# Kernel optimization log

Hardware: AMD Instinct MI355X
Metric: run time of the kernel (lower is better)

Reference implementation:

```python
import jax, jax.numpy as jnp
import numpy as np

B, N, D = 64, 4096, 256      # batch, num_inputs, in_features
S, K, H = 11, 128, 256       # num_slots, slot_size, mlp_hidden_size
ITERS = 3
EPS = 1e-6
LN_EPS = 1e-5


def layer_norm(x, w, b):
    m = jnp.mean(x, axis=-1, keepdims=True)
    v = jnp.mean(jnp.square(x - m), axis=-1, keepdims=True)
    return (x - m) * jax.lax.rsqrt(v + LN_EPS) * w + b


def setup_inputs() -> dict:
    key = jax.random.key(0)
    ks = jax.random.split(key, 24)
    rn = lambda i, shape, sc=1.0: jax.random.normal(ks[i], shape, jnp.float32) * sc
    p = 0.05  # param init scale
    return {
        "inputs": rn(0, (B, N, D)),
        "slots_init": rn(1, (B, S, K)),
        "slots_mu": rn(2, (1, 1, K), p),
        "slots_log_sigma": rn(3, (1, 1, K), p),
        "ln_in_w": 1.0 + rn(4, (D,), p), "ln_in_b": rn(5, (D,), p),
        "ln_slot_w": 1.0 + rn(6, (K,), p), "ln_slot_b": rn(7, (K,), p),
        "ln_mlp_w": 1.0 + rn(8, (K,), p), "ln_mlp_b": rn(9, (K,), p),
        "Wq": rn(10, (K, K), p),
        "Wk": rn(11, (K, D), p),
        "Wv": rn(12, (K, D), p),
        "w_ih": rn(13, (3 * K, K), p), "w_hh": rn(14, (3 * K, K), p),
        "b_ih": rn(15, (3 * K,), p), "b_hh": rn(16, (3 * K,), p),
        "mlp_w1": rn(17, (H, K), p), "mlp_b1": rn(18, (H,), p),
        "mlp_w2": rn(19, (K, H), p), "mlp_b2": rn(20, (K,), p),
    }


def reference(inputs, slots_init, slots_mu, slots_log_sigma,
              ln_in_w, ln_in_b, ln_slot_w, ln_slot_b, ln_mlp_w, ln_mlp_b,
              Wq, Wk, Wv, w_ih, w_hh, b_ih, b_hh,
              mlp_w1, mlp_b1, mlp_w2, mlp_b2):
    x = layer_norm(inputs, ln_in_w, ln_in_b)            # [B,N,D]
    k = jnp.einsum('bnd,kd->bnk', x, Wk)                # [B,N,K]
    v = jnp.einsum('bnd,kd->bnk', x, Wv)                # [B,N,K]
    slots = slots_mu + jnp.exp(slots_log_sigma) * slots_init  # [B,S,K]
    scale = K ** -0.5
    for _ in range(ITERS):
        slots_prev = slots
        sn = layer_norm(slots, ln_slot_w, ln_slot_b)
        q = jnp.einsum('bsk,jk->bsj', sn, Wq)           # [B,S,K]
        logits = scale * jnp.einsum('bnk,bsk->bns', k, q)  # [B,N,S]
        attn = jax.nn.softmax(logits, axis=-1) + EPS    # softmax over slots
        attn = attn / jnp.sum(attn, axis=1, keepdims=True)  # renorm over inputs
        updates = jnp.einsum('bns,bnk->bsk', attn, v)   # [B,S,K]
        # GRUCell: input=updates, hidden=slots_prev
        gi = jnp.einsum('bsk,jk->bsj', updates, w_ih) + b_ih     # [B,S,3K]
        gh = jnp.einsum('bsk,jk->bsj', slots_prev, w_hh) + b_hh  # [B,S,3K]
        i_r, i_z, i_n = jnp.split(gi, 3, axis=-1)
        h_r, h_z, h_n = jnp.split(gh, 3, axis=-1)
        r = jax.nn.sigmoid(i_r + h_r)
        z = jax.nn.sigmoid(i_z + h_z)
        n = jnp.tanh(i_n + r * h_n)
        slots = (1.0 - z) * n + z * slots_prev
        m = layer_norm(slots, ln_mlp_w, ln_mlp_b)
        hid = jax.nn.relu(jnp.einsum('bsk,hk->bsh', m, mlp_w1) + mlp_b1)
        slots = slots + jnp.einsum('bsh,kh->bsk', hid, mlp_w2) + mlp_b2
    return slots
```

## Files before the change

kernel.cpp:

```cpp
#include <hip/hip_runtime.h>
#include <hip/hip_bf16.h>
#include <cstdint>
#include <cstddef>

#define B_ 64
#define N_ 4096
#define D_ 256
#define S_ 11
#define K_ 128
#define H_ 256
#define ITERS_ 3
#define EPS_ 1e-6f
#define LN_EPS_ 1e-5f
#define SCALE_ 0.08838834764831845f
#define NCH_ 16

typedef __bf16 bf16x8 __attribute__((ext_vector_type(8)));
typedef float  f32x4  __attribute__((ext_vector_type(4)));

__device__ __forceinline__ unsigned short f2bu(float f) {
  __bf16 h = (__bf16)f;
  return __builtin_bit_cast(unsigned short, h);
}
__device__ __forceinline__ unsigned int pk2(float a, float b) {
  return (unsigned int)f2bu(a) | ((unsigned int)f2bu(b) << 16);
}

__global__ __launch_bounds__(256) void kprep(const float* __restrict__ Wk,
                                             const float* __restrict__ Wv,
                                             const float* __restrict__ lnw,
                                             const float* __restrict__ lnb,
                                             unsigned short* __restrict__ W2pk,
                                             float* __restrict__ c1c2,
                                             const float* __restrict__ si,
                                             const float* __restrict__ mu,
                                             const float* __restrict__ ls,
                                             float* __restrict__ slots,
                                             const float* __restrict__ w_ih,
                                             const float* __restrict__ w_hh,
                                             float* __restrict__ wTih,
                                             float* __restrict__ wThh,
                                             const float* __restrict__ w1,
                                             float* __restrict__ w1T,
                                             const float* __restrict__ w2,
                                             float* __restrict__ w2T,
                                             const float* __restrict__ Wq,
                                             float* __restrict__ WqT) {
  int bid = blockIdx.x, t = threadIdx.x;
  if (bid < 32) {
    int f = bid * 256 + t;
    int ln_ = f & 63, jj = (f >> 6) & 3, kk2 = (f >> 8) & 1, kt = (f >> 9) & 3, ww = f >> 11;
    int row = ww * 64 + jj * 16 + (ln_ & 15);
    int col = kt * 64 + kk2 * 32 + (ln_ >> 4) * 8;
    const float* src = (row < 128) ? (Wk + row * 256 + col) : (Wv + (row - 128) * 256 + col);
    float4 a = *(const float4*)src;
    float4 b = *(const float4*)(src + 4);
    float4 l0 = *(const float4*)(lnw + col);
    float4 l1 = *(const float4*)(lnw + col + 4);
    a.x *= l0.x; a.y *= l0.y; a.z *= l0.z; a.w *= l0.w;
    b.x *= l1.x; b.y *= l1.y; b.z *= l1.z; b.w *= l1.w;
    uint4 u;
    u.x = pk2(a.x, a.y); u.y = pk2(a.z, a.w); u.z = pk2(b.x, b.y); u.w = pk2(b.z, b.w);
    *(uint4*)(W2pk + (size_t)f * 8) = u;
  } else if (bid < 384) {
    int i = (bid - 32) * 256 + t;
    int k = i & 127;
    slots[i] = mu[k] + __expf(ls[k]) * si[i];
  } else if (bid < 576) {
    int i = (bid - 384) * 256 + t;
    int r = i >> 7, c = i & 127;
    wTih[c * 384 + r] = w_ih[i];
  } else if (bid < 768) {
    int i = (bid - 576) * 256 + t;
    int r = i >> 7, c = i & 127;
    wThh[c * 384 + r] = w_hh[i];
  } else if (bid < 896) {
    int i = (bid - 768) * 256 + t;
    int r = i >> 7, c = i & 127;
    w1T[c * 256 + r] = w1[i];
  } else if (bid < 1024) {
    int i = (bid - 896) * 256 + t;
    int r = i >> 8, c = i & 255;
    w2T[c * 128 + r] = w2[i];
  } else if (bid < 1088) {
    int i = (bid - 1024) * 256 + t;
    int r = i >> 7, c = i & 127;
    WqT[c * 128 + r] = Wq[i];
  } else {
    int j = t;
    const float* wrow = (j < 128) ? (Wk + j * 256) : (Wv + (j - 128) * 256);
    float c1 = 0.f, c2 = 0.f;
    for (int d = 0; d < 256; d++) {
      float wv = wrow[d];
      c1 += lnb[d] * wv;
      c2 += lnw[d] * wv;
    }
    c1c2[2 * j] = c1;
    c1c2[2 * j + 1] = c2;
  }
}

__global__ __launch_bounds__(256) void k12_lngemm(const float* __restrict__ x,
                                                  const float* __restrict__ c1c2,
                                                  const unsigned short* __restrict__ W2pk,
                                                  unsigned short* __restrict__ k_frag,
                                                  unsigned short* __restrict__ v_frag) {
  __shared__ char smem[32768];
  __shared__ float2 mu_a[64];
  __shared__ float2 ccs[256];
  const int t = threadIdx.x;
  const int lane = t & 63, w = t >> 6;
  const long rowg0 = (long)blockIdx.x * 64;

  ccs[t] = ((const float2*)c1c2)[t];

  bf16x8 bA[4], bB[4];
  auto loadB = [&](int kt, int kk, bf16x8* dst) {
#pragma unroll
    for (int jl = 0; jl < 4; jl++)
      dst[jl] = *(const bf16x8*)(W2pk +
          (size_t)((w << 11) | (kt << 9) | (kk << 8) | (jl << 6) | lane) * 8);
  };
  loadB(0, 0, bA);

  {
    const float* xb = x + (rowg0 + w * 16) * 256 + lane * 4;
#pragma unroll
    for (int rr = 0; rr < 16; rr++) {
      float4 xv = *(const float4*)(xb + rr * 256);
      int r = w * 16 + rr;
      uint2 pk;
      pk.x = pk2(xv.x, xv.y);
      pk.y = pk2(xv.z, xv.w);
      *(uint2*)(smem + r * 512 + (((lane >> 1) ^ (r & 7)) << 4) + ((lane & 1) << 3)) = pk;
    }
  }
  __syncthreads();

  {
    const int sr = t >> 2, squad = t & 3;
    float s = 0.f, ss = 0.f;
#pragma unroll
    for (int c8 = 0; c8 < 8; c8++) {
      bf16x8 v = *(const bf16x8*)(smem + sr * 512 + ((((squad * 8 + c8) ^ (sr & 7))) << 4));
#pragma unroll
      for (int e = 0; e < 8; e++) {
        float f = (float)v[e];
        s += f; ss += f * f;
      }
    }
    s += __shfl_xor(s, 1);  s += __shfl_xor(s, 2);
    ss += __shfl_xor(ss, 1); ss += __shfl_xor(ss, 2);
    if (squad == 0) {
      float m = s * (1.f / 256.f);
      float var = ss * (1.f / 256.f) - m * m;
      float2 ma; ma.x = m; ma.y = rsqrtf(var + LN_EPS_);
      mu_a[sr] = ma;
    }
  }

  f32x4 acc[4][4] = {};
#pragma unroll
  for (int sstep = 0; sstep < 8; sstep++) {
    const int kt = sstep >> 1, kk = sstep & 1;
    const bf16x8* cur = (sstep & 1) ? bB : bA;
    bf16x8* nxt = (sstep & 1) ? bA : bB;
    if (sstep < 7) loadB((sstep + 1) >> 1, (sstep + 1) & 1, nxt);
    bf16x8 xf[4];
#pragma unroll
    for (int i = 0; i < 4; i++) {
      int row = i * 16 + (lane & 15);
      int slot = (kt * 8 + kk * 4 + (lane >> 4)) ^ (lane & 7);
      xf[i] = *(const bf16x8*)(smem + row * 512 + (slot << 4));
    }
    if (w < 2) {
#pragma unroll
      for (int i = 0; i < 4; i++)
#pragma unroll
        for (int jl = 0; jl < 4; jl++)
          acc[i][jl] = __builtin_amdgcn_mfma_f32_16x16x32_bf16(cur[jl], xf[i], acc[i][jl], 0, 0, 0);
    } else {
#pragma unroll
      for (int i = 0; i < 4; i++)
#pragma unroll
        for (int jl = 0; jl < 4; jl++)
          acc[i][jl] = __builtin_amdgcn_mfma_f32_16x16x32_bf16(xf[i], cur[jl], acc[i][jl], 0, 0, 0);
    }
  }
  __syncthreads();

  const int ll = lane & 15, lh = lane >> 4;
  if (w < 2) {
    float2 ccr[4][4];
#pragma unroll
    for (int jl = 0; jl < 4; jl++) {
      int jg = w * 4 + jl;
#pragma unroll
      for (int reg = 0; reg < 4; reg++) ccr[jl][reg] = ccs[jg * 16 + lh * 4 + reg];
    }
#pragma unroll
    for (int i = 0; i < 4; i++) {
      float2 ma = mu_a[i * 16 + ll];
#pragma unroll
      for (int jl = 0; jl < 4; jl++) {
        int jg = w * 4 + jl;
        float v0 = ma.y * (acc[i][jl][0] - ma.x * ccr[jl][0].y) + ccr[jl][0].x;
        float v1 = ma.y * (acc[i][jl][1] - ma.x * ccr[jl][1].y) + ccr[jl][1].x;
        float v2 = ma.y * (acc[i][jl][2] - ma.x * ccr[jl][2].y) + ccr[jl][2].x;
        float v3 = ma.y * (acc[i][jl][3] - ma.x * ccr[jl][3].y) + ccr[jl][3].x;
        uint2 pk;
        pk.x = pk2(v0, v1); pk.y = pk2(v2, v3);
        size_t chunk = ((size_t)(rowg0 >> 4) + i) * 4 + (jg >> 1);
        int off = (ll + 16 * ((jg & 1) * 2 + (lh >> 1))) * 8 + (lh & 1) * 4;
        *(uint2*)(k_frag + chunk * 512 + off) = pk;
      }
    }
  } else {
    float2 cj[4];
#pragma unroll
    for (int jl = 0; jl < 4; jl++) cj[jl] = ccs[128 + (w - 2) * 64 + jl * 16 + ll];
#pragma unroll
    for (int i = 0; i < 4; i++) {
      float2 ma0 = mu_a[i * 16 + lh * 4 + 0];
      float2 ma1 = mu_a[i * 16 + lh * 4 + 1];
      float2 ma2 = mu_a[i * 16 + lh * 4 + 2];
      float2 ma3 = mu_a[i * 16 + lh * 4 + 3];
#pragma unroll
      for (int jl = 0; jl < 4; jl++) {
        float v0 = ma0.y * (acc[i][jl][0] - ma0.x * cj[jl].y) + cj[jl].x;
        float v1 = ma1.y * (acc[i][jl][1] - ma1.x * cj[jl].y) + cj[jl].x;
        float v2 = ma2.y * (acc[i][jl][2] - ma2.x * cj[jl].y) + cj[jl].x;
        float v3 = ma3.y * (acc[i][jl][3] - ma3.x * cj[jl].y) + cj[jl].x;
        uint2 pk;
        pk.x = pk2(v0, v1); pk.y = pk2(v2, v3);
        size_t chunk = ((size_t)(rowg0 >> 5) + (i >> 1)) * 8 + (w - 2) * 4 + jl;
        int off = (ll + 16 * ((i & 1) * 2 + (lh >> 1))) * 8 + (lh & 1) * 4;
        *(uint2*)(v_frag + chunk * 512 + off) = pk;
      }
    }
  }
}

__device__ __forceinline__ float redsum128(float v, float* red2) {
#pragma unroll
  for (int o = 1; o < 64; o <<= 1) v += __shfl_xor(v, o);
  __syncthreads();
  if ((threadIdx.x & 63) == 0) red2[threadIdx.x >> 6] = v;
  __syncthreads();
  return red2[0] + red2[1];
}

__global__ __launch_bounds__(128) void k3_q(const float* __restrict__ slots,
                                            const float* __restrict__ lw,
                                            const float* __restrict__ lb,
                                            const float* __restrict__ WqT,
                                            float* __restrict__ q) {
  int bs = blockIdx.x;
  int j = threadIdx.x;
  __shared__ float sn[128];
  __shared__ float red2[2];
  float x = slots[(size_t)bs * 128 + j];
  float sum = redsum128(x, red2);
  float sq  = redsum128(x * x, red2);
  float mean = sum * (1.f / 128.f);
  float var  = sq * (1.f / 128.f) - mean * mean;
  float v = (x - mean) * rsqrtf(var + LN_EPS_) * lw[j] + lb[j];
  sn[j] = v;
  __syncthreads();
  float acc = 0.f;
#pragma unroll 8
  for (int kk = 0; kk < 128; kk++) acc += sn[kk] * WqT[kk * 128 + j];
  q[(size_t)bs * 128 + j] = acc;
}

__global__ __launch_bounds__(256) void k45_attn(const unsigned short* __restrict__ k_frag,
                                                const unsigned short* __restrict__ v_frag,
                                                const float* __restrict__ qbuf,
                                                float* __restrict__ num_part,
                                                float* __restrict__ den_part) {
  __shared__ unsigned short att[16 * 264];
  __shared__ float redd[4][16];
  const int t = threadIdx.x;
  const int lane = t & 63, w = t >> 6;
  const int b = blockIdx.x >> 4, chunk = blockIdx.x & (NCH_ - 1);

  int sqi = lane & 15; if (sqi > 10) sqi = 10;
  const float* qp = qbuf + ((size_t)b * S_ + sqi) * 128 + (lane >> 4) * 8;
  bf16x8 qf[4];
#pragma unroll
  for (int ks = 0; ks < 4; ks++) {
    float4 q0 = *(const float4*)(qp + ks * 32);
    float4 q1 = *(const float4*)(qp + ks * 32 + 4);
    uint4 uu;
    uu.x = pk2(q0.x, q0.y); uu.y = pk2(q0.z, q0.w);
    uu.z = pk2(q1.x, q1.y); uu.w = pk2(q1.z, q1.w);
    qf[ks] = __builtin_bit_cast(bf16x8, uu);
  }
  const bool dead = (lane & 15) >= 11;
  float dden = 0.f;

#pragma unroll
  for (int u = 0; u < 4; u++) {
    size_t g = (size_t)b * 256 + chunk * 16 + w * 4 + u;
    f32x4 lg = {0.f, 0.f, 0.f, 0.f};
#pragma unroll
    for (int ks = 0; ks < 4; ks++) {
      bf16x8 af = *(const bf16x8*)(k_frag + (g * 4 + ks) * 512 + lane * 8);
      lg = __builtin_amdgcn_mfma_f32_16x16x32_bf16(af, qf[ks], lg, 0, 0, 0);
    }
    float l0 = dead ? -1e30f : lg[0] * SCALE_;
    float l1 = dead ? -1e30f : lg[1] * SCALE_;
    float l2 = dead ? -1e30f : lg[2] * SCALE_;
    float l3 = dead ? -1e30f : lg[3] * SCALE_;
    float m0 = l0, m1 = l1, m2 = l2, m3 = l3;
#pragma unroll
    for (int o = 1; o < 16; o <<= 1) {
      m0 = fmaxf(m0, __shfl_xor(m0, o)); m1 = fmaxf(m1, __shfl_xor(m1, o));
      m2 = fmaxf(m2, __shfl_xor(m2, o)); m3 = fmaxf(m3, __shfl_xor(m3, o));
    }
    float e0 = __expf(l0 - m0), e1 = __expf(l1 - m1);
    float e2 = __expf(l2 - m2), e3 = __expf(l3 - m3);
    float t0 = e0, t1 = e1, t2 = e2, t3 = e3;
#pragma unroll
    for (int o = 1; o < 16; o <<= 1) {
      t0 += __shfl_xor(t0, o); t1 += __shfl_xor(t1, o);
      t2 += __shfl_xor(t2, o); t3 += __shfl_xor(t3, o);
    }
    float a0 = e0 / t0 + EPS_, a1 = e1 / t1 + EPS_;
    float a2 = e2 / t2 + EPS_, a3 = e3 / t3 + EPS_;
    dden += a0 + a1 + a2 + a3;
    uint2 pk;
    pk.x = pk2(a0, a1); pk.y = pk2(a2, a3);
    int s = lane & 15;
    int nn = w * 64 + u * 16 + (lane >> 4) * 4;
    *(uint2*)((char*)att + s * 528 + nn * 2) = pk;
  }
  dden += __shfl_xor(dden, 16);
  dden += __shfl_xor(dden, 32);
  if (lane < 16) redd[w][lane] = dden;
  __syncthreads();
  if (t < S_)
    den_part[((size_t)b * NCH_ + chunk) * S_ + t] =
        redd[0][t] + redd[1][t] + redd[2][t] + redd[3][t];

  f32x4 acc[2] = {};
#pragma unroll
  for (int ks = 0; ks < 8; ks++) {
    bf16x8 pa = *(const bf16x8*)((const char*)att + (lane & 15) * 528 +
                                 (ks * 32 + (lane >> 4) * 8) * 2);
    size_t nb = (size_t)b * 128 + chunk * 8 + ks;
#pragma unroll
    for (int j = 0; j < 2; j++) {
      bf16x8 vb = *(const bf16x8*)(v_frag + (nb * 8 + (w * 2 + j)) * 512 + lane * 8);
      acc[j] = __builtin_amdgcn_mfma_f32_16x16x32_bf16(pa, vb, acc[j], 0, 0, 0);
    }
  }
#pragma unroll
  for (int j = 0; j < 2; j++)
#pragma unroll
    for (int r = 0; r < 4; r++) {
      int s = (lane >> 4) * 4 + r;
      if (s < S_) {
        int k = w * 32 + j * 16 + (lane & 15);
        num_part[(((size_t)b * NCH_ + chunk) * S_ + s) * 128 + k] = acc[j][r];
      }
    }
}

__global__ __launch_bounds__(256) void k63_final(const float* __restrict__ num_part,
                                                 const float* __restrict__ den_part,
                                                 float* __restrict__ slots,
                                                 const float* __restrict__ wTih,
                                                 const float* __restrict__ wThh,
                                                 const float* __restrict__ b_ih,
                                                 const float* __restrict__ b_hh,
                                                 const float* __restrict__ lmw,
                                                 const float* __restrict__ lmb,
                                                 const float* __restrict__ w1T,
                                                 const float* __restrict__ bb1,
                                                 const float* __restrict__ w2T,
                                                 const float* __restrict__ bb2,
                                                 const float* __restrict__ lsw,
                                                 const float* __restrict__ lsb,
                                                 const float* __restrict__ WqT,
                                                 float* __restrict__ qbuf,
                                                 float* __restrict__ outp,
                                                 int cq, int wout) {
  int bs = blockIdx.x;
  int b = bs / S_, s = bs % S_;
  int t = threadIdx.x;
  int j = t & 127, half = t >> 7;
  __shared__ float u[128], h[128], gp[3][128], m[128], hid[256], sjs[128], op[128];
  __shared__ float ns[128], snq[128];
  __shared__ float red2a[2], red2b[2];

  if (half == 0) {
    float den = 0.f;
#pragma unroll
    for (int c = 0; c < NCH_; c++) den += den_part[((size_t)b * NCH_ + c) * S_ + s];
    float uj = 0.f;
#pragma unroll
    for (int c = 0; c < NCH_; c++) uj += num_part[(((size_t)b * NCH_ + c) * S_ + s) * 128 + j];
    u[j] = uj / den;
  } else {
    h[j] = slots[((size_t)b * S_ + s) * 128 + j];
  }
  __syncthreads();

  {
    const float* wT = half ? wThh : wTih;
    const float* sv = half ? h : u;
    float g0 = 0.f, g1 = 0.f, g2 = 0.f;
#pragma unroll 8
    for (int kk = 0; kk < 128; kk++) {
      float vv = sv[kk];
      const float* wr = wT + kk * 384;
      g0 += wr[j] * vv; g1 += wr[128 + j] * vv; g2 += wr[256 + j] * vv;
    }
    if (half) { gp[0][j] = g0; gp[1][j] = g1; gp[2][j] = g2; }
    __syncthreads();
    float sj = 0.f;
    if (half == 0) {
      float gr = g0 + b_ih[j]       + gp[0][j] + b_hh[j];
      float gz = g1 + b_ih[128 + j] + gp[1][j] + b_hh[128 + j];
      float r = 1.f / (1.f + __expf(-gr));
      float z = 1.f / (1.f + __expf(-gz));
      float nn = tanhf(g2 + b_ih[256 + j] + r * (gp[2][j] + b_hh[256 + j]));
      sj = (1.f - z) * nn + z * h[j];
      sjs[j] = sj;
    }
    float sv2 = sj, sq2 = sj * sj;
#pragma unroll
    for (int o = 1; o < 64; o <<= 1) { sv2 += __shfl_xor(sv2, o); sq2 += __shfl_xor(sq2, o); }
    if (half == 0 && (t & 63) == 0) { red2a[t >> 6] = sv2; red2b[t >> 6] = sq2; }
    __syncthreads();
    float mean = (red2a[0] + red2a[1]) * (1.f / 128.f);
    float var  = (red2b[0] + red2b[1]) * (1.f / 128.f) - mean * mean;
    float rstd = rsqrtf(var + LN_EPS_);
    if (half == 0) m[j] = (sj - mean) * rstd * lmw[j] + lmb[j];
  }
  __syncthreads();

  {
    float a = bb1[t];
#pragma unroll 8
    for (int kk = 0; kk < 128; kk++) a += w1T[kk * 256 + t] * m[kk];
    hid[t] = fmaxf(a, 0.f);
  }
  __syncthreads();

  {
    const float* w2p = w2T + (size_t)half * 128 * 128 + j;
    const float* hp = hid + half * 128;
    float o2 = 0.f;
#pragma unroll 8
    for (int q2 = 0; q2 < 128; q2++) o2 += w2p[q2 * 128] * hp[q2];
    if (half) op[j] = o2;
    __syncthreads();
    if (half == 0) {
      float ov = sjs[j] + bb2[j] + o2 + op[j];
      slots[((size_t)b * S_ + s) * 128 + j] = ov;
      if (wout) outp[((size_t)b * S_ + s) * 128 + j] = ov;
      ns[j] = ov;
    }
  }
  __syncthreads();

  if (cq) {
    float vv = (half == 0) ? ns[j] : 0.f;
    float s1 = vv, s2 = vv * vv;
#pragma unroll
    for (int o = 1; o < 64; o <<= 1) { s1 += __shfl_xor(s1, o); s2 += __shfl_xor(s2, o); }
    if (half == 0 && (t & 63) == 0) { red2a[t >> 6] = s1; red2b[t >> 6] = s2; }
    __syncthreads();
    float mean = (red2a[0] + red2a[1]) * (1.f / 128.f);
    float var  = (red2b[0] + red2b[1]) * (1.f / 128.f) - mean * mean;
    float rstd = rsqrtf(var + LN_EPS_);
    if (half == 0) snq[j] = (ns[j] - mean) * rstd * lsw[j] + lsb[j];
    __syncthreads();
    const float* wq = WqT + (size_t)half * 64 * 128;
    const float* sp = snq + half * 64;
    float qv = 0.f;
#pragma unroll 8
    for (int kk = 0; kk < 64; kk++) qv += wq[kk * 128 + j] * sp[kk];
    if (half) op[j] = qv;
    __syncthreads();
    if (half == 0) qbuf[(size_t)bs * 128 + j] = qv + op[j];
  }
}

extern "C" void kernel_launch(void* const* d_in, const int* in_sizes, int n_in,
                              void* d_out, int out_size, void* d_ws, size_t ws_size,
                              hipStream_t stream) {
  (void)in_sizes; (void)n_in; (void)out_size; (void)ws_size;
  const float* inputs     = (const float*)d_in[0];
  const float* slots_init = (const float*)d_in[1];
  const float* slots_mu   = (const float*)d_in[2];
  const float* slots_ls   = (const float*)d_in[3];
  const float* ln_in_w    = (const float*)d_in[4];
  const float* ln_in_b    = (const float*)d_in[5];
  const float* ln_slot_w  = (const float*)d_in[6];
  const float* ln_slot_b  = (const float*)d_in[7];
  const float* ln_mlp_w   = (const float*)d_in[8];
  const float* ln_mlp_b   = (const float*)d_in[9];
  const float* Wq         = (const float*)d_in[10];
  const float* Wk         = (const float*)d_in[11];
  const float* Wv         = (const float*)d_in[12];
  const float* w_ih       = (const float*)d_in[13];
  const float* w_hh       = (const float*)d_in[14];
  const float* b_ih       = (const float*)d_in[15];
  const float* b_hh       = (const float*)d_in[16];
  const float* mlp_w1     = (const float*)d_in[17];
  const float* mlp_b1     = (const float*)d_in[18];
  const float* mlp_w2     = (const float*)d_in[19];
  const float* mlp_b2     = (const float*)d_in[20];

  uintptr_t p = (uintptr_t)d_ws;
  auto carve = [&](size_t bytes) -> void* {
    void* r = (void*)p;
    p += (bytes + 255) & ~(size_t)255;
    return r;
  };
  unsigned short* k_frag = (unsigned short*)carve((size_t)B_ * N_ * K_ * 2);
  unsigned short* v_frag = (unsigned short*)carve((size_t)B_ * K_ * N_ * 2);
  unsigned short* W2pk   = (unsigned short*)carve((size_t)256 * 256 * 2);
  float* c1c2  = (float*)carve((size_t)256 * 2 * 4);
  float* wTih  = (float*)carve((size_t)128 * 384 * 4);
  float* wThh  = (float*)carve((size_t)128 * 384 * 4);
  float* w1T   = (float*)carve((size_t)128 * 256 * 4);
  float* w2T   = (float*)carve((size_t)256 * 128 * 4);
  float* WqT   = (float*)carve((size_t)128 * 128 * 4);
  float* qbuf     = (float*)carve((size_t)B_ * S_ * K_ * 4);
  float* slots    = (float*)carve((size_t)B_ * S_ * K_ * 4);
  float* den_part = (float*)carve((size_t)B_ * NCH_ * S_ * 4);
  float* num_part = (float*)carve((size_t)B_ * NCH_ * S_ * K_ * 4);

  kprep<<<1089, 256, 0, stream>>>(Wk, Wv, ln_in_w, ln_in_b, W2pk, c1c2,
                                  slots_init, slots_mu, slots_ls, slots,
                                  w_ih, w_hh, wTih, wThh, mlp_w1, w1T, mlp_w2, w2T,
                                  Wq, WqT);
  k12_lngemm<<<(B_ * N_) / 64, 256, 0, stream>>>(inputs, c1c2, W2pk, k_frag, v_frag);
  k3_q<<<B_ * S_, 128, 0, stream>>>(slots, ln_slot_w, ln_slot_b, WqT, qbuf);

  for (int it = 0; it < ITERS_; ++it) {
    k45_attn<<<B_ * NCH_, 256, 0, stream>>>(k_frag, v_frag, qbuf, num_part, den_part);
    k63_final<<<B_ * S_, 256, 0, stream>>>(num_part, den_part, slots,
                                           wTih, wThh, b_ih, b_hh,
                                           ln_mlp_w, ln_mlp_b,
                                           w1T, mlp_b1, w2T, mlp_b2,
                                           ln_slot_w, ln_slot_b, WqT, qbuf,
                                           (float*)d_out,
                                           (it < ITERS_ - 1) ? 1 : 0,
                                           (it == ITERS_ - 1) ? 1 : 0);
  }
}
```

Measured before the change: 259.0 us.

## Restructure LN+KV projection GEMM: x in registers, weights staged via global_load_lds

The LayerNorm+K/V projection kernel now keeps each wave's 16 input rows directly in registers as bf16 MFMA fragments and computes LN statistics with cross-lane shuffles. This removes the shared-memory round trip for x. Each wave now computes all 256 output columns for its own rows. Weight fragments are repacked per k-step and double-buffered in LDS through async global_load_lds, shared by all four waves, replacing per-wave direct global weight loads. This aims to cut LDS traffic and redundant weight fetches and to raise occupancy via launch bounds, at the cost of more accumulator registers and a barrier per k-step.

```diff
diff --git a/kernel.cpp b/kernel.cpp
--- a/kernel.cpp
+++ b/kernel.cpp
@@ -24,6 +24,10 @@
 }
 __device__ __forceinline__ unsigned int pk2(float a, float b) {
   return (unsigned int)f2bu(a) | ((unsigned int)f2bu(b) << 16);
+}
+__device__ __forceinline__ void gl16(const void* g, void* l) {
+  __builtin_amdgcn_global_load_lds((const __attribute__((address_space(1))) void*)g,
+                                   (__attribute__((address_space(3))) void*)l, 16, 0, 0);
 }
 
 __global__ __launch_bounds__(256) void kprep(const float* __restrict__ Wk,
@@ -49,10 +53,10 @@
   int bid = blockIdx.x, t = threadIdx.x;
   if (bid < 32) {
     int f = bid * 256 + t;
-    int ln_ = f & 63, jj = (f >> 6) & 3, kk2 = (f >> 8) & 1, kt = (f >> 9) & 3, ww = f >> 11;
-    int row = ww * 64 + jj * 16 + (ln_ & 15);
-    int col = kt * 64 + kk2 * 32 + (ln_ >> 4) * 8;
-    const float* src = (row < 128) ? (Wk + row * 256 + col) : (Wv + (row - 128) * 256 + col);
+    int ln_ = f & 63, frag = (f >> 6) & 15, kst = f >> 10;
+    int row = (frag & 7) * 16 + (ln_ & 15);
+    int col = kst * 32 + (ln_ >> 4) * 8;
+    const float* src = ((frag < 8) ? Wk : Wv) + row * 256 + col;
     float4 a = *(const float4*)src;
     float4 b = *(const float4*)(src + 4);
     float4 l0 = *(const float4*)(lnw + col);
@@ -100,143 +104,113 @@
   }
 }
 
-__global__ __launch_bounds__(256) void k12_lngemm(const float* __restrict__ x,
-                                                  const float* __restrict__ c1c2,
-                                                  const unsigned short* __restrict__ W2pk,
-                                                  unsigned short* __restrict__ k_frag,
-                                                  unsigned short* __restrict__ v_frag) {
-  __shared__ char smem[32768];
+__global__ __launch_bounds__(256, 4) void k12_lngemm(const float* __restrict__ x,
+                                                     const float* __restrict__ c1c2,
+                                                     const unsigned short* __restrict__ W2pk,
+                                                     unsigned short* __restrict__ k_frag,
+                                                     unsigned short* __restrict__ v_frag) {
+  __shared__ __attribute__((aligned(16))) char wbuf[2][16384];
+  __shared__ float2 ccs[256];
   __shared__ float2 mu_a[64];
-  __shared__ float2 ccs[256];
   const int t = threadIdx.x;
   const int lane = t & 63, w = t >> 6;
+  const int ll = lane & 15, lh = lane >> 4;
   const long rowg0 = (long)blockIdx.x * 64;
 
+  const float* xp = x + (rowg0 + w * 16 + ll) * 256 + lh * 8;
+  float4 xa[16];
+#pragma unroll
+  for (int kst = 0; kst < 8; kst++) {
+    xa[2 * kst]     = *(const float4*)(xp + kst * 32);
+    xa[2 * kst + 1] = *(const float4*)(xp + kst * 32 + 4);
+  }
+
+  auto stageW = [&](int kst) {
+    const unsigned short* src = W2pk + (size_t)kst * 8192;
+#pragma unroll
+    for (int i = 0; i < 4; i++) {
+      int cb = i * 4 + w;
+      gl16(src + cb * 512 + lane * 8, wbuf[kst & 1] + cb * 1024);
+    }
+  };
+  stageW(0);
+
   ccs[t] = ((const float2*)c1c2)[t];
 
-  bf16x8 bA[4], bB[4];
-  auto loadB = [&](int kt, int kk, bf16x8* dst) {
-#pragma unroll
-    for (int jl = 0; jl < 4; jl++)
-      dst[jl] = *(const bf16x8*)(W2pk +
-          (size_t)((w << 11) | (kt << 9) | (kk << 8) | (jl << 6) | lane) * 8);
-  };
-  loadB(0, 0, bA);
-
+  bf16x8 xr[8];
+  float s = 0.f, ss = 0.f;
+#pragma unroll
+  for (int kst = 0; kst < 8; kst++) {
+    float4 a = xa[2 * kst], b = xa[2 * kst + 1];
+    s  += a.x + a.y + a.z + a.w + b.x + b.y + b.z + b.w;
+    ss += a.x * a.x + a.y * a.y + a.z * a.z + a.w * a.w
+        + b.x * b.x + b.y * b.y + b.z * b.z + b.w * b.w;
+    uint4 u;
+    u.x = pk2(a.x, a.y); u.y = pk2(a.z, a.w); u.z = pk2(b.x, b.y); u.w = pk2(b.z, b.w);
+    xr[kst] = __builtin_bit_cast(bf16x8, u);
+  }
+  s  += __shfl_xor(s, 16);  s  += __shfl_xor(s, 32);
+  ss += __shfl_xor(ss, 16); ss += __shfl_xor(ss, 32);
+  const float mu_own = s * (1.f / 256.f);
+  const float rs_own = rsqrtf(ss * (1.f / 256.f) - mu_own * mu_own + LN_EPS_);
+  if (lh == 0) {
+    float2 ma; ma.x = mu_own; ma.y = rs_own;
+    mu_a[w * 16 + ll] = ma;
+  }
+  __syncthreads();
+
+  f32x4 acck[8] = {};
+  f32x4 accv[8] = {};
+#pragma unroll
+  for (int kst = 0; kst < 8; kst++) {
+    if (kst < 7) stageW(kst + 1);
+    const char* wb = wbuf[kst & 1];
+#pragma unroll
+    for (int jg = 0; jg < 8; jg++) {
+      bf16x8 wf = *(const bf16x8*)(wb + jg * 1024 + lane * 16);
+      acck[jg] = __builtin_amdgcn_mfma_f32_16x16x32_bf16(wf, xr[kst], acck[jg], 0, 0, 0);
+    }
+#pragma unroll
+    for (int jv = 0; jv < 8; jv++) {
+      bf16x8 wf = *(const bf16x8*)(wb + (8 + jv) * 1024 + lane * 16);
+      accv[jv] = __builtin_amdgcn_mfma_f32_16x16x32_bf16(xr[kst], wf, accv[jv], 0, 0, 0);
+    }
+    if (kst < 7) __syncthreads();
+  }
+
+#pragma unroll
+  for (int jg = 0; jg < 8; jg++) {
+    float2 c0 = ccs[jg * 16 + lh * 4 + 0];
+    float2 c1 = ccs[jg * 16 + lh * 4 + 1];
+    float2 c2 = ccs[jg * 16 + lh * 4 + 2];
+    float2 c3 = ccs[jg * 16 + lh * 4 + 3];
+    float v0 = rs_own * (acck[jg][0] - mu_own * c0.y) + c0.x;
+    float v1 = rs_own * (acck[jg][1] - mu_own * c1.y) + c1.x;
+    float v2 = rs_own * (acck[jg][2] - mu_own * c2.y) + c2.x;
+    float v3 = rs_own * (acck[jg][3] - mu_own * c3.y) + c3.x;
+    uint2 pk;
+    pk.x = pk2(v0, v1); pk.y = pk2(v2, v3);
+    size_t chunk = ((size_t)(rowg0 >> 4) + w) * 4 + (jg >> 1);
+    int off = (ll + 16 * ((jg & 1) * 2 + (lh >> 1))) * 8 + (lh & 1) * 4;
+    *(uint2*)(k_frag + chunk * 512 + off) = pk;
+  }
   {
-    const float* xb = x + (rowg0 + w * 16) * 256 + lane * 4;
-#pragma unroll
-    for (int rr = 0; rr < 16; rr++) {
-      float4 xv = *(const float4*)(xb + rr * 256);
-      int r = w * 16 + rr;
+    float2 ma0 = mu_a[w * 16 + lh * 4 + 0];
+    float2 ma1 = mu_a[w * 16 + lh * 4 + 1];
+    float2 ma2 = mu_a[w * 16 + lh * 4 + 2];
+    float2 ma3 = mu_a[w * 16 + lh * 4 + 3];
+#pragma unroll
+    for (int jv = 0; jv < 8; jv++) {
+      float2 cc = ccs[128 + jv * 16 + ll];
+      float v0 = ma0.y * (accv[jv][0] - ma0.x * cc.y) + cc.x;
+      float v1 = ma1.y * (accv[jv][1] - ma1.x * cc.y) + cc.x;
+      float v2 = ma2.y * (accv[jv][2] - ma2.x * cc.y) + cc.x;
+      float v3 = ma3.y * (accv[jv][3] - ma3.x * cc.y) + cc.x;
       uint2 pk;
-      pk.x = pk2(xv.x, xv.y);
-      pk.y = pk2(xv.z, xv.w);
-      *(uint2*)(smem + r * 512 + (((lane >> 1) ^ (r & 7)) << 4) + ((lane & 1) << 3)) = pk;
-    }
-  }
-  __syncthreads();
-
-  {
-    const int sr = t >> 2, squad = t & 3;
-    float s = 0.f, ss = 0.f;
-#pragma unroll
-    for (int c8 = 0; c8 < 8; c8++) {
-      bf16x8 v = *(const bf16x8*)(smem + sr * 512 + ((((squad * 8 + c8) ^ (sr & 7))) << 4));
-#pragma unroll
-      for (int e = 0; e < 8; e++) {
-        float f = (float)v[e];
-        s += f; ss += f * f;
-      }
-    }
-    s += __shfl_xor(s, 1);  s += __shfl_xor(s, 2);
-    ss += __shfl_xor(ss, 1); ss += __shfl_xor(ss, 2);
-    if (squad == 0) {
-      float m = s * (1.f / 256.f);
-      float var = ss * (1.f / 256.f) - m * m;
-      float2 ma; ma.x = m; ma.y = rsqrtf(var + LN_EPS_);
-      mu_a[sr] = ma;
-    }
-  }
-
-  f32x4 acc[4][4] = {};
-#pragma unroll
-  for (int sstep = 0; sstep < 8; sstep++) {
-    const int kt = sstep >> 1, kk = sstep & 1;
-    const bf16x8* cur = (sstep & 1) ? bB : bA;
-    bf16x8* nxt = (sstep & 1) ? bA : bB;
-    if (sstep < 7) loadB((sstep + 1) >> 1, (sstep + 1) & 1, nxt);
-    bf16x8 xf[4];
-#pragma unroll
-    for (int i = 0; i < 4; i++) {
-      int row = i * 16 + (lane & 15);
-      int slot = (kt * 8 + kk * 4 + (lane >> 4)) ^ (lane & 7);
-      xf[i] = *(const bf16x8*)(smem + row * 512 + (slot << 4));
-    }
-    if (w < 2) {
-#pragma unroll
-      for (int i = 0; i < 4; i++)
-#pragma unroll
-        for (int jl = 0; jl < 4; jl++)
-          acc[i][jl] = __builtin_amdgcn_mfma_f32_16x16x32_bf16(cur[jl], xf[i], acc[i][jl], 0, 0, 0);
-    } else {
-#pragma unroll
-      for (int i = 0; i < 4; i++)
-#pragma unroll
-        for (int jl = 0; jl < 4; jl++)
-          acc[i][jl] = __builtin_amdgcn_mfma_f32_16x16x32_bf16(xf[i], cur[jl], acc[i][jl], 0, 0, 0);
-    }
-  }
-  __syncthreads();
-
-  const int ll = lane & 15, lh = lane >> 4;
-  if (w < 2) {
-    float2 ccr[4][4];
-#pragma unroll
-    for (int jl = 0; jl < 4; jl++) {
-      int jg = w * 4 + jl;
-#pragma unroll
-      for (int reg = 0; reg < 4; reg++) ccr[jl][reg] = ccs[jg * 16 + lh * 4 + reg];
-    }
-#pragma unroll
-    for (int i = 0; i < 4; i++) {
-      float2 ma = mu_a[i * 16 + ll];
-#pragma unroll
-      for (int jl = 0; jl < 4; jl++) {
-        int jg = w * 4 + jl;
-        float v0 = ma.y * (acc[i][jl][0] - ma.x * ccr[jl][0].y) + ccr[jl][0].x;
-        float v1 = ma.y * (acc[i][jl][1] - ma.x * ccr[jl][1].y) + ccr[jl][1].x;
-        float v2 = ma.y * (acc[i][jl][2] - ma.x * ccr[jl][2].y) + ccr[jl][2].x;
-        float v3 = ma.y * (acc[i][jl][3] - ma.x * ccr[jl][3].y) + ccr[jl][3].x;
-        uint2 pk;
-        pk.x = pk2(v0, v1); pk.y = pk2(v2, v3);
-        size_t chunk = ((size_t)(rowg0 >> 4) + i) * 4 + (jg >> 1);
-        int off = (ll + 16 * ((jg & 1) * 2 + (lh >> 1))) * 8 + (lh & 1) * 4;
-        *(uint2*)(k_frag + chunk * 512 + off) = pk;
-      }
-    }
-  } else {
-    float2 cj[4];
-#pragma unroll
-    for (int jl = 0; jl < 4; jl++) cj[jl] = ccs[128 + (w - 2) * 64 + jl * 16 + ll];
-#pragma unroll
-    for (int i = 0; i < 4; i++) {
-      float2 ma0 = mu_a[i * 16 + lh * 4 + 0];
-      float2 ma1 = mu_a[i * 16 + lh * 4 + 1];
-      float2 ma2 = mu_a[i * 16 + lh * 4 + 2];
-      float2 ma3 = mu_a[i * 16 + lh * 4 + 3];
-#pragma unroll
-      for (int jl = 0; jl < 4; jl++) {
-        float v0 = ma0.y * (acc[i][jl][0] - ma0.x * cj[jl].y) + cj[jl].x;
-        float v1 = ma1.y * (acc[i][jl][1] - ma1.x * cj[jl].y) + cj[jl].x;
-        float v2 = ma2.y * (acc[i][jl][2] - ma2.x * cj[jl].y) + cj[jl].x;
-        float v3 = ma3.y * (acc[i][jl][3] - ma3.x * cj[jl].y) + cj[jl].x;
-        uint2 pk;
-        pk.x = pk2(v0, v1); pk.y = pk2(v2, v3);
-        size_t chunk = ((size_t)(rowg0 >> 5) + (i >> 1)) * 8 + (w - 2) * 4 + jl;
-        int off = (ll + 16 * ((i & 1) * 2 + (lh >> 1))) * 8 + (lh & 1) * 4;
-        *(uint2*)(v_frag + chunk * 512 + off) = pk;
-      }
+      pk.x = pk2(v0, v1); pk.y = pk2(v2, v3);
+      size_t chunk = ((size_t)(rowg0 >> 5) + (w >> 1)) * 8 + jv;
+      int off = (ll + 16 * ((w & 1) * 2 + (lh >> 1))) * 8 + (lh & 1) * 4;
+      *(uint2*)(v_frag + chunk * 512 + off) = pk;
     }
   }
 }
```

Result: slower. 296.6 us (+14.5%).
